# Kernel optimization log

Hardware: AMD Instinct MI355X
Metric: run time of the kernel (lower is better)

Reference implementation:

```python
import jax, jax.numpy as jnp
import numpy as np

N = 50000          # num nodes
E = 800000         # num edges
D = 128            # dim_in == embed_dim
MAX_NODES = 4      # hard-coded in SortConv.__init__
EPS = 1e-5


def setup_inputs() -> dict:
    key = jax.random.key(0)
    ks = jax.random.split(key, 16)
    inp = {
        'x': jax.random.normal(ks[0], (N, D), jnp.float32),
        'edge_index': jax.random.randint(ks[1], (2, E), 0, N, jnp.int32),
    }
    for i in range(2):
        o = 2 + 6 * i
        W = jax.random.normal(ks[o], (D, D), jnp.float32) * (2.0 / (D + D)) ** 0.5
        W = W / jnp.linalg.norm(W, axis=1, keepdims=True)   # reset_parameters row-normalization
        inp[f'W{i}'] = W
        inp[f'b{i}'] = jnp.zeros((D,), jnp.float32)
        inp[f'cw{i}'] = jax.random.normal(ks[o + 1], (MAX_NODES,), jnp.float32) * (2.0 / (MAX_NODES + 1)) ** 0.5
        inp[f'cb{i}'] = jnp.zeros((1,), jnp.float32)
        inp[f'a{i}'] = jax.random.uniform(ks[o + 2], (1,), jnp.float32, -1.0, 1.0)  # LinearCombination scalar
        inp[f'g{i}'] = jnp.ones((D,), jnp.float32)
        inp[f'be{i}'] = jnp.zeros((D,), jnp.float32)
        inp[f'blank{i}'] = jnp.zeros((D,), jnp.float32)      # learnable blank vector
    return inp


def sort_conv(x, edge_index, blank, W, b, cw, cb, a):
    n, d = x.shape
    e = edge_index.shape[1]
    src, dst = edge_index[0], edge_index[1]
    msgs = x[src]                                            # [E, D] raw messages (lin_project not applied to messages)
    order = jnp.argsort(dst)                                 # stable sort by destination (index_sort)
    dst_s = dst[order]
    counts = jax.ops.segment_sum(jnp.ones((e,), jnp.int32), dst, num_segments=n + 1)
    starts = jnp.concatenate([jnp.zeros((1,), jnp.int32), jnp.cumsum(counts)[:-1].astype(jnp.int32)])
    pos = jnp.arange(e, dtype=jnp.int32) - starts[dst_s]     # rank within each neighborhood
    slot = jnp.where(pos < MAX_NODES, pos, MAX_NODES)        # overflow edges -> trash slot (to_dense_batch truncation)
    dense = jnp.zeros((n + 1, MAX_NODES + 1, d), x.dtype).at[dst_s, slot].set(msgs[order])
    mask = jnp.zeros((n + 1, MAX_NODES + 1), bool).at[dst_s, slot].set(True)
    dense, mask = dense[:, :MAX_NODES], mask[:, :MAX_NODES]  # [N+1, 4, D], [N+1, 4]
    blank_p = W @ blank + b                                  # lin_project applied only to blank vector
    filled = dense + (~mask)[..., None].astype(x.dtype) * blank_p
    srt = jnp.sort(filled, axis=1)                           # per-feature sort over neighbor slots
    out = jnp.einsum('nmd,m->nd', srt, cw) + cb              # vector collapse: Linear(max_nodes, 1)
    node_out, blank_new = out[:-1], out[-1]                  # last row = all-blank graph -> new blank
    return a * x + node_out, a * blank + blank_new           # LinearCombination combine (num_repeats=1)


def batch_norm(h, g, be):
    mu = h.mean(0)
    var = h.var(0)
    return (h - mu) / jnp.sqrt(var + EPS) * g + be


def reference(x, edge_index, W0, b0, cw0, cb0, a0, g0, be0, blank0,
              W1, b1, cw1, cb1, a1, g1, be1, blank1):
    layers = [(W0, b0, cw0, cb0, a0, g0, be0, blank0),
              (W1, b1, cw1, cb1, a1, g1, be1, blank1)]
    for (W, b, cw, cb, a, g, be, blank) in layers:
        h, _ = sort_conv(x, edge_index, blank, W, b, cw, cb, a)
        h = batch_norm(h, g, be)
        x = x + h                                            # residual connection
    return x
```

## Files before the change

kernel.cpp:

```cpp
#include <hip/hip_runtime.h>
#include <climits>

constexpr int N_NODES = 50000;
constexpr int N_EDGES = 800000;
constexpr int DIM     = 128;
constexpr int DIM4    = DIM / 4;
constexpr float BN_EPS = 1e-5f;

constexpr int EMPTY = 0x7F7F7F7F;

constexpr int NC = 16;
constexpr int EC = 16;
constexpr int NODES_PER_NC = N_NODES / NC;
constexpr int EDGES_PER_EC = N_EDGES / EC;
constexpr int E4_PER_EC    = EDGES_PER_EC / 4;
constexpr int SEL_THREADS  = 1024;

constexpr int NODES_PER_ITER  = 8;
constexpr int CONV_ITERS      = 2;
constexpr int NODES_PER_BLOCK = NODES_PER_ITER * CONV_ITERS;
constexpr int CONV_GRID = N_NODES / NODES_PER_BLOCK;

constexpr int NBUCKETS = 64;
constexpr int NB_MERGE = (N_NODES + 255) / 256;

__device__ inline float4 f4min(float4 a, float4 b) {
    return make_float4(fminf(a.x,b.x), fminf(a.y,b.y), fminf(a.z,b.z), fminf(a.w,b.w));
}
__device__ inline float4 f4max(float4 a, float4 b) {
    return make_float4(fmaxf(a.x,b.x), fmaxf(a.y,b.y), fmaxf(a.z,b.z), fmaxf(a.w,b.w));
}
__device__ inline float4 f4add(float4 a, float4 b) {
    return make_float4(a.x+b.x, a.y+b.y, a.z+b.z, a.w+b.w);
}
__device__ inline float4 f4fma(float s, float4 v, float4 acc) {
    return make_float4(fmaf(s,v.x,acc.x), fmaf(s,v.y,acc.y), fmaf(s,v.z,acc.z), fmaf(s,v.w,acc.w));
}

__global__ __launch_bounds__(SEL_THREADS)
void select_stageA_kernel(const int* __restrict__ dst,
                          int* __restrict__ tables) {
    __shared__ int slot[NODES_PER_NC * 4];
    const int nc = blockIdx.x & (NC - 1);
    const int ec = blockIdx.x >> 4;
    const int t  = threadIdx.x;

    for (int i = t; i < NODES_PER_NC * 4; i += SEL_THREADS) slot[i] = EMPTY;
    __syncthreads();

    const int r0 = nc * NODES_PER_NC;
    const int4* __restrict__ dst4 = (const int4*)dst;
    const int base4 = ec * E4_PER_EC;
    for (int i = t; i < E4_PER_EC; i += SEL_THREADS) {
        const int4 d = dst4[base4 + i];
        const int ebase = 4 * (base4 + i);
        #define TRY_INS(comp, off) {                                        \
            unsigned n_ = (unsigned)((comp) - r0);                          \
            if (n_ < (unsigned)NODES_PER_NC) {                              \
                int cur_ = ebase + (off);                                   \
                _Pragma("unroll")                                           \
                for (int j_ = 0; j_ < 4; ++j_) {                            \
                    int old_ = atomicMin(&slot[4 * n_ + j_], cur_);         \
                    if (old_ == EMPTY) break;                               \
                    cur_ = max(cur_, old_);                                 \
                } } }
        TRY_INS(d.x, 0); TRY_INS(d.y, 1); TRY_INS(d.z, 2); TRY_INS(d.w, 3);
        #undef TRY_INS
    }
    __syncthreads();

    int4* __restrict__ out = (int4*)tables + (size_t)ec * N_NODES + r0;
    const int4* __restrict__ sl4 = (const int4*)slot;
    for (int n = t; n < NODES_PER_NC; n += SEL_THREADS) out[n] = sl4[n];
}

__global__ __launch_bounds__(256)
void select_stageB_kernel(const int* __restrict__ tables,
                          const int* __restrict__ src,
                          int4* __restrict__ srcs4,
                          float* __restrict__ stats_part,
                          const float* __restrict__ W0, const float* __restrict__ b0,
                          const float* __restrict__ bl0,
                          const float* __restrict__ W1, const float* __restrict__ b1,
                          const float* __restrict__ bl1,
                          float* __restrict__ bp) {
    const int t = threadIdx.x;

    if (blockIdx.x >= NB_MERGE) {
        if (t < DIM) {
            int l = blockIdx.x - NB_MERGE;
            const float* W  = l ? W1  : W0;
            const float* b  = l ? b1  : b0;
            const float* bl = l ? bl1 : bl0;
            float s = 0.f;
            #pragma unroll 8
            for (int j = 0; j < DIM; ++j) s += W[t * DIM + j] * bl[j];
            bp[l * DIM + t] = s + b[t];
        }
        return;
    }

    const int gid = blockIdx.x * 256 + t;
    if (gid < 2 * NBUCKETS * 256) stats_part[gid] = 0.f;

    const int v = gid;
    if (v >= N_NODES) return;

    int b0_ = EMPTY, b1_ = EMPTY, b2_ = EMPTY, b3_ = EMPTY;
    #pragma unroll
    for (int ec = 0; ec < EC; ++ec) {
        const int4 c = ((const int4*)tables)[(size_t)ec * N_NODES + v];
        if (c.x >= b3_) continue;
        #define INS(val) {                                          \
            int x_ = (val);                                         \
            if (x_ < b3_) { b3_ = x_;                               \
                int tm;                                             \
                if (b3_ < b2_) { tm = b2_; b2_ = b3_; b3_ = tm; }   \
                if (b2_ < b1_) { tm = b1_; b1_ = b2_; b2_ = tm; }   \
                if (b1_ < b0_) { tm = b0_; b0_ = b1_; b1_ = tm; } } }
        INS(c.x); INS(c.y); INS(c.z); INS(c.w);
        #undef INS
    }
    int4 o;
    o.x = (b0_ < N_EDGES) ? src[b0_] : -1;
    o.y = (b1_ < N_EDGES) ? src[b1_] : -1;
    o.z = (b2_ < N_EDGES) ? src[b2_] : -1;
    o.w = (b3_ < N_EDGES) ? src[b3_] : -1;
    srcs4[v] = o;
}

__global__ __launch_bounds__(256)
void conv_stats_kernel(const float* __restrict__ x,
                       const int4* __restrict__ srcs4,
                       const float* __restrict__ bp,
                       const float* __restrict__ cw,
                       const float* __restrict__ cb,
                       const float* __restrict__ a,
                       float* __restrict__ h,
                       float* __restrict__ stats_part) {
    const int t    = threadIdx.x;
    const int d4   = t & (DIM4 - 1);
    const int nsub = t >> 5;

    const float4* __restrict__ x4 = (const float4*)x;
    float4*       __restrict__ h4 = (float4*)h;

    const float aa = a[0];
    const float c0 = cw[0], c1 = cw[1], c2 = cw[2], c3 = cw[3];
    const float cbv = cb[0];
    const float4 bpv = ((const float4*)bp)[d4];

    const int v0 = blockIdx.x * NODES_PER_BLOCK + nsub;
    const int v1 = v0 + NODES_PER_ITER;

    const int4 s0 = srcs4[v0];
    const int4 s1 = srcs4[v1];

    float4 g00 = x4[(size_t)max(s0.x, 0) * DIM4 + d4];
    float4 g01 = x4[(size_t)max(s0.y, 0) * DIM4 + d4];
    float4 g02 = x4[(size_t)max(s0.z, 0) * DIM4 + d4];
    float4 g03 = x4[(size_t)max(s0.w, 0) * DIM4 + d4];
    float4 g10 = x4[(size_t)max(s1.x, 0) * DIM4 + d4];
    float4 g11 = x4[(size_t)max(s1.y, 0) * DIM4 + d4];
    float4 g12 = x4[(size_t)max(s1.z, 0) * DIM4 + d4];
    float4 g13 = x4[(size_t)max(s1.w, 0) * DIM4 + d4];
    float4 xv0 = x4[(size_t)v0 * DIM4 + d4];
    float4 xv1 = x4[(size_t)v1 * DIM4 + d4];

    float4 s  = make_float4(0.f, 0.f, 0.f, 0.f);
    float4 s2 = make_float4(0.f, 0.f, 0.f, 0.f);

    #define CSWAP4(p, q) { float4 lo = f4min(p, q); float4 hi = f4max(p, q); p = lo; q = hi; }
    {
        float4 m0 = (s0.x >= 0) ? g00 : bpv;
        float4 m1 = (s0.y >= 0) ? g01 : bpv;
        float4 m2 = (s0.z >= 0) ? g02 : bpv;
        float4 m3 = (s0.w >= 0) ? g03 : bpv;
        CSWAP4(m0, m1); CSWAP4(m2, m3); CSWAP4(m0, m2); CSWAP4(m1, m3); CSWAP4(m1, m2);
        float4 hv = make_float4(cbv, cbv, cbv, cbv);
        hv = f4fma(c0, m0, hv);
        hv = f4fma(c1, m1, hv);
        hv = f4fma(c2, m2, hv);
        hv = f4fma(c3, m3, hv);
        hv = f4fma(aa, xv0, hv);
        h4[(size_t)v0 * DIM4 + d4] = hv;
        s  = f4add(s, hv);
        s2 = f4add(s2, make_float4(hv.x*hv.x, hv.y*hv.y, hv.z*hv.z, hv.w*hv.w));
    }
    {
        float4 m0 = (s1.x >= 0) ? g10 : bpv;
        float4 m1 = (s1.y >= 0) ? g11 : bpv;
        float4 m2 = (s1.z >= 0) ? g12 : bpv;
        float4 m3 = (s1.w >= 0) ? g13 : bpv;
        CSWAP4(m0, m1); CSWAP4(m2, m3); CSWAP4(m0, m2); CSWAP4(m1, m3); CSWAP4(m1, m2);
        float4 hv = make_float4(cbv, cbv, cbv, cbv);
        hv = f4fma(c0, m0, hv);
        hv = f4fma(c1, m1, hv);
        hv = f4fma(c2, m2, hv);
        hv = f4fma(c3, m3, hv);
        hv = f4fma(aa, xv1, hv);
        h4[(size_t)v1 * DIM4 + d4] = hv;
        s  = f4add(s, hv);
        s2 = f4add(s2, make_float4(hv.x*hv.x, hv.y*hv.y, hv.z*hv.z, hv.w*hv.w));
    }
    #undef CSWAP4

    s.x  += __shfl_down(s.x, 32);  s.y  += __shfl_down(s.y, 32);
    s.z  += __shfl_down(s.z, 32);  s.w  += __shfl_down(s.w, 32);
    s2.x += __shfl_down(s2.x, 32); s2.y += __shfl_down(s2.y, 32);
    s2.z += __shfl_down(s2.z, 32); s2.w += __shfl_down(s2.w, 32);

    __shared__ float4 ls[4][32];
    __shared__ float4 ls2[4][32];
    const int wave = t >> 6;
    const int lane = t & 63;
    if (lane < 32) { ls[wave][lane] = s; ls2[wave][lane] = s2; }
    __syncthreads();
    if (t < 32) {
        float* bucket = stats_part + (size_t)(blockIdx.x & (NBUCKETS - 1)) * 256;
        float4 fs  = f4add(f4add(ls[0][t],  ls[1][t]),  f4add(ls[2][t],  ls[3][t]));
        float4 fs2 = f4add(f4add(ls2[0][t], ls2[1][t]), f4add(ls2[2][t], ls2[3][t]));
        atomicAdd(&bucket[4*t + 0], fs.x);
        atomicAdd(&bucket[4*t + 1], fs.y);
        atomicAdd(&bucket[4*t + 2], fs.z);
        atomicAdd(&bucket[4*t + 3], fs.w);
        atomicAdd(&bucket[DIM + 4*t + 0], fs2.x);
        atomicAdd(&bucket[DIM + 4*t + 1], fs2.y);
        atomicAdd(&bucket[DIM + 4*t + 2], fs2.z);
        atomicAdd(&bucket[DIM + 4*t + 3], fs2.w);
    }
}

__global__ void reduce_finalize_kernel(const float* __restrict__ stats_part,
                                       float* __restrict__ final) {
    __shared__ float acc[256];
    int t = threadIdx.x;
    float s = 0.f;
    #pragma unroll 8
    for (int k = 0; k < NBUCKETS; ++k) s += stats_part[k * 256 + t];
    acc[t] = s;
    __syncthreads();
    if (t < 128) {
        constexpr float invN = 1.0f / (float)N_NODES;
        float mu = acc[t] * invN;
        float iv = rsqrtf(acc[128 + t] * invN - mu * mu + BN_EPS);
        final[t]       = mu;
        final[128 + t] = iv;
    }
}

__global__ void bn_apply_kernel(const float* __restrict__ xin,
                                const float* __restrict__ h,
                                const float* __restrict__ final,
                                const float* __restrict__ g,
                                const float* __restrict__ be,
                                float* __restrict__ xout) {
    int idx = blockIdx.x * blockDim.x + threadIdx.x;
    constexpr int TOTAL4 = N_NODES * DIM4;
    if (idx >= TOTAL4) return;
    int d4 = idx & (DIM4 - 1);

    float4 mu = ((const float4*)final)[d4];
    float4 iv = ((const float4*)(final + DIM))[d4];
    float4 hv = ((const float4*)h)[idx];
    float4 xv = ((const float4*)xin)[idx];
    float4 gv = ((const float4*)g)[d4];
    float4 bv = ((const float4*)be)[d4];

    float4 o;
    o.x = xv.x + (hv.x - mu.x) * iv.x * gv.x + bv.x;
    o.y = xv.y + (hv.y - mu.y) * iv.y * gv.y + bv.y;
    o.z = xv.z + (hv.z - mu.z) * iv.z * gv.z + bv.z;
    o.w = xv.w + (hv.w - mu.w) * iv.w * gv.w + bv.w;
    ((float4*)xout)[idx] = o;
}

extern "C" void kernel_launch(void* const* d_in, const int* in_sizes, int n_in,
                              void* d_out, int out_size, void* d_ws, size_t ws_size,
                              hipStream_t stream) {
    const float* x0  = (const float*)d_in[0];
    const int*   ei  = (const int*)d_in[1];
    const int*   src = ei;
    const int*   dst = ei + N_EDGES;

    const float* W[2]; const float* b[2]; const float* cw[2]; const float* cb[2];
    const float* a[2]; const float* g[2]; const float* be[2]; const float* blank[2];
    for (int i = 0; i < 2; ++i) {
        int o = 2 + 8 * i;
        W[i]     = (const float*)d_in[o + 0];
        b[i]     = (const float*)d_in[o + 1];
        cw[i]    = (const float*)d_in[o + 2];
        cb[i]    = (const float*)d_in[o + 3];
        a[i]     = (const float*)d_in[o + 4];
        g[i]     = (const float*)d_in[o + 5];
        be[i]    = (const float*)d_in[o + 6];
        blank[i] = (const float*)d_in[o + 7];
    }

    char* ws = (char*)d_ws;
    int*   srcs       = (int*)ws;
    float* h          = (float*)(srcs + 4 * N_NODES);
    int*   tables     = (int*)h;
    float* stats_part = h + (size_t)N_NODES * DIM;
    float* final_     = stats_part + 2 * NBUCKETS * 256;
    float* bp         = final_ + 512;

    float* xout = (float*)d_out;

    select_stageA_kernel<<<NC * EC, SEL_THREADS, 0, stream>>>(dst, tables);
    select_stageB_kernel<<<NB_MERGE + 2, 256, 0, stream>>>(
        tables, src, (int4*)srcs, stats_part,
        W[0], b[0], blank[0], W[1], b[1], blank[1], bp);

    for (int l = 0; l < 2; ++l) {
        const float* xin = (l == 0) ? x0 : xout;
        float* sp = stats_part + (size_t)l * NBUCKETS * 256;
        conv_stats_kernel<<<CONV_GRID, 256, 0, stream>>>(
            xin, (const int4*)srcs, bp + l * DIM, cw[l], cb[l], a[l], h, sp);
        reduce_finalize_kernel<<<1, 256, 0, stream>>>(sp, final_ + l * 256);
        bn_apply_kernel<<<(N_NODES * DIM4 + 255) / 256, 256, 0, stream>>>(
            xin, h, final_ + l * 256, g[l], be[l], xout);
    }
}
```

Before: 209.7 us.

## Fuse conv, BN statistics and BN apply into one persistent kernel with grid barrier

Replaces the three per-layer kernels (conv+stats, reduce/finalize, bn_apply) with a single persistent kernel of 1024 blocks. Each block keeps its conv outputs in LDS across several tiles. The last block to arrive at an atomic counter reduces the statistics, then releases the other blocks, which apply batch norm straight from LDS. This removes the global write and re-read of the h intermediate and two launches per layer. The trade-off is higher LDS use per block and a spin-wait grid barrier that deadlocks if the 1024 blocks cannot all be resident at once.

```diff
diff --git a/kernel.cpp b/kernel.cpp
--- a/kernel.cpp
+++ b/kernel.cpp
@@ -1,5 +1,4 @@
 #include <hip/hip_runtime.h>
-#include <climits>
 
 constexpr int N_NODES = 50000;
 constexpr int N_EDGES = 800000;
@@ -16,13 +15,16 @@
 constexpr int E4_PER_EC    = EDGES_PER_EC / 4;
 constexpr int SEL_THREADS  = 1024;
 
-constexpr int NODES_PER_ITER  = 8;
-constexpr int CONV_ITERS      = 2;
-constexpr int NODES_PER_BLOCK = NODES_PER_ITER * CONV_ITERS;
-constexpr int CONV_GRID = N_NODES / NODES_PER_BLOCK;
-
-constexpr int NBUCKETS = 64;
+constexpr int NBUCKETS = 32;
 constexpr int NB_MERGE = (N_NODES + 255) / 256;
+
+constexpr int PGRID = 1024;
+constexpr int NODES_PER_TILE = 8;
+constexpr int CONV_GRID = N_NODES / NODES_PER_TILE;
+constexpr int TILES = (CONV_GRID + PGRID - 1) / PGRID;
+
+constexpr int STATS_WORDS = 2 * NBUCKETS * 256;
+constexpr int ZERO_WORDS  = STATS_WORDS + 4;
 
 __device__ inline float4 f4min(float4 a, float4 b) {
     return make_float4(fminf(a.x,b.x), fminf(a.y,b.y), fminf(a.z,b.z), fminf(a.w,b.w));
@@ -101,7 +103,7 @@
     }
 
     const int gid = blockIdx.x * 256 + t;
-    if (gid < 2 * NBUCKETS * 256) stats_part[gid] = 0.f;
+    if (gid < ZERO_WORDS) stats_part[gid] = 0.f;
 
     const int v = gid;
     if (v >= N_NODES) return;
@@ -129,79 +131,70 @@
     srcs4[v] = o;
 }
 
-__global__ __launch_bounds__(256)
-void conv_stats_kernel(const float* __restrict__ x,
-                       const int4* __restrict__ srcs4,
-                       const float* __restrict__ bp,
-                       const float* __restrict__ cw,
-                       const float* __restrict__ cb,
-                       const float* __restrict__ a,
-                       float* __restrict__ h,
-                       float* __restrict__ stats_part) {
+__global__ __launch_bounds__(256, 4)
+void conv_bn_fused_kernel(const float* __restrict__ xin,
+                          const int4* __restrict__ srcs4,
+                          const float* __restrict__ bp,
+                          const float* __restrict__ cw,
+                          const float* __restrict__ cb,
+                          const float* __restrict__ a,
+                          const float* __restrict__ g,
+                          const float* __restrict__ be,
+                          float* __restrict__ stats_part,
+                          float* __restrict__ final_,
+                          int* __restrict__ bar,
+                          float* __restrict__ xout) {
+    __shared__ float4 hv_lds[TILES][256];
+    __shared__ float4 ls[4][32];
+    __shared__ float4 ls2[4][32];
+    __shared__ float acc[256];
+    __shared__ int is_last;
+
     const int t    = threadIdx.x;
+    const int bid  = blockIdx.x;
     const int d4   = t & (DIM4 - 1);
     const int nsub = t >> 5;
 
-    const float4* __restrict__ x4 = (const float4*)x;
-    float4*       __restrict__ h4 = (float4*)h;
+    const float4* __restrict__ x4  = (const float4*)xin;
+    float4*       __restrict__ xo4 = (float4*)xout;
 
     const float aa = a[0];
     const float c0 = cw[0], c1 = cw[1], c2 = cw[2], c3 = cw[3];
     const float cbv = cb[0];
     const float4 bpv = ((const float4*)bp)[d4];
 
-    const int v0 = blockIdx.x * NODES_PER_BLOCK + nsub;
-    const int v1 = v0 + NODES_PER_ITER;
-
-    const int4 s0 = srcs4[v0];
-    const int4 s1 = srcs4[v1];
-
-    float4 g00 = x4[(size_t)max(s0.x, 0) * DIM4 + d4];
-    float4 g01 = x4[(size_t)max(s0.y, 0) * DIM4 + d4];
-    float4 g02 = x4[(size_t)max(s0.z, 0) * DIM4 + d4];
-    float4 g03 = x4[(size_t)max(s0.w, 0) * DIM4 + d4];
-    float4 g10 = x4[(size_t)max(s1.x, 0) * DIM4 + d4];
-    float4 g11 = x4[(size_t)max(s1.y, 0) * DIM4 + d4];
-    float4 g12 = x4[(size_t)max(s1.z, 0) * DIM4 + d4];
-    float4 g13 = x4[(size_t)max(s1.w, 0) * DIM4 + d4];
-    float4 xv0 = x4[(size_t)v0 * DIM4 + d4];
-    float4 xv1 = x4[(size_t)v1 * DIM4 + d4];
-
     float4 s  = make_float4(0.f, 0.f, 0.f, 0.f);
     float4 s2 = make_float4(0.f, 0.f, 0.f, 0.f);
 
     #define CSWAP4(p, q) { float4 lo = f4min(p, q); float4 hi = f4max(p, q); p = lo; q = hi; }
-    {
-        float4 m0 = (s0.x >= 0) ? g00 : bpv;
-        float4 m1 = (s0.y >= 0) ? g01 : bpv;
-        float4 m2 = (s0.z >= 0) ? g02 : bpv;
-        float4 m3 = (s0.w >= 0) ? g03 : bpv;
-        CSWAP4(m0, m1); CSWAP4(m2, m3); CSWAP4(m0, m2); CSWAP4(m1, m3); CSWAP4(m1, m2);
-        float4 hv = make_float4(cbv, cbv, cbv, cbv);
-        hv = f4fma(c0, m0, hv);
-        hv = f4fma(c1, m1, hv);
-        hv = f4fma(c2, m2, hv);
-        hv = f4fma(c3, m3, hv);
-        hv = f4fma(aa, xv0, hv);
-        h4[(size_t)v0 * DIM4 + d4] = hv;
-        s  = f4add(s, hv);
-        s2 = f4add(s2, make_float4(hv.x*hv.x, hv.y*hv.y, hv.z*hv.z, hv.w*hv.w));
-    }
-    {
-        float4 m0 = (s1.x >= 0) ? g10 : bpv;
-        float4 m1 = (s1.y >= 0) ? g11 : bpv;
-        float4 m2 = (s1.z >= 0) ? g12 : bpv;
-        float4 m3 = (s1.w >= 0) ? g13 : bpv;
-        CSWAP4(m0, m1); CSWAP4(m2, m3); CSWAP4(m0, m2); CSWAP4(m1, m3); CSWAP4(m1, m2);
-        float4 hv = make_float4(cbv, cbv, cbv, cbv);
-        hv = f4fma(c0, m0, hv);
-        hv = f4fma(c1, m1, hv);
-        hv = f4fma(c2, m2, hv);
-        hv = f4fma(c3, m3, hv);
-        hv = f4fma(aa, xv1, hv);
-        h4[(size_t)v1 * DIM4 + d4] = hv;
-        s  = f4add(s, hv);
-        s2 = f4add(s2, make_float4(hv.x*hv.x, hv.y*hv.y, hv.z*hv.z, hv.w*hv.w));
+    #pragma unroll
+    for (int k = 0; k < TILES; ++k) {
+        const int tile = k * PGRID + bid;
+        if (tile < CONV_GRID) {
+            const int v = tile * NODES_PER_TILE + nsub;
+            const int4 i0 = srcs4[v];
+
+            float4 g00 = x4[(size_t)max(i0.x, 0) * DIM4 + d4];
+            float4 g01 = x4[(size_t)max(i0.y, 0) * DIM4 + d4];
+            float4 g02 = x4[(size_t)max(i0.z, 0) * DIM4 + d4];
+            float4 g03 = x4[(size_t)max(i0.w, 0) * DIM4 + d4];
+            float4 xv  = x4[(size_t)v * DIM4 + d4];
+
+            float4 m0 = (i0.x >= 0) ? g00 : bpv;
+            float4 m1 = (i0.y >= 0) ? g01 : bpv;
+            float4 m2 = (i0.z >= 0) ? g02 : bpv;
+            float4 m3 = (i0.w >= 0) ? g03 : bpv;
+            CSWAP4(m0, m1); CSWAP4(m2, m3); CSWAP4(m0, m2); CSWAP4(m1, m3); CSWAP4(m1, m2);
+            float4 hv = make_float4(cbv, cbv, cbv, cbv);
+            hv = f4fma(c0, m0, hv);
+            hv = f4fma(c1, m1, hv);
+            hv = f4fma(c2, m2, hv);
+            hv = f4fma(c3, m3, hv);
+            hv = f4fma(aa, xv, hv);
+            hv_lds[k][t] = hv;
+            s  = f4add(s, hv);
+            s2 = f4add(s2, make_float4(hv.x*hv.x, hv.y*hv.y, hv.z*hv.z, hv.w*hv.w));
+        }
     }
     #undef CSWAP4
 
@@ -210,14 +203,12 @@
     s2.x += __shfl_down(s2.x, 32); s2.y += __shfl_down(s2.y, 32);
     s2.z += __shfl_down(s2.z, 32); s2.w += __shfl_down(s2.w, 32);
 
-    __shared__ float4 ls[4][32];
-    __shared__ float4 ls2[4][32];
     const int wave = t >> 6;
     const int lane = t & 63;
     if (lane < 32) { ls[wave][lane] = s; ls2[wave][lane] = s2; }
     __syncthreads();
     if (t < 32) {
-        float* bucket = stats_part + (size_t)(blockIdx.x & (NBUCKETS - 1)) * 256;
+        float* bucket = stats_part + (size_t)(bid & (NBUCKETS - 1)) * 256;
         float4 fs  = f4add(f4add(ls[0][t],  ls[1][t]),  f4add(ls[2][t],  ls[3][t]));
         float4 fs2 = f4add(f4add(ls2[0][t], ls2[1][t]), f4add(ls2[2][t], ls2[3][t]));
         atomicAdd(&bucket[4*t + 0], fs.x);
@@ -229,50 +220,70 @@
         atomicAdd(&bucket[DIM + 4*t + 2], fs2.z);
         atomicAdd(&bucket[DIM + 4*t + 3], fs2.w);
     }
-}
-
-__global__ void reduce_finalize_kernel(const float* __restrict__ stats_part,
-                                       float* __restrict__ final) {
-    __shared__ float acc[256];
-    int t = threadIdx.x;
-    float s = 0.f;
-    #pragma unroll 8
-    for (int k = 0; k < NBUCKETS; ++k) s += stats_part[k * 256 + t];
-    acc[t] = s;
-    __syncthreads();
-    if (t < 128) {
-        constexpr float invN = 1.0f / (float)N_NODES;
-        float mu = acc[t] * invN;
-        float iv = rsqrtf(acc[128 + t] * invN - mu * mu + BN_EPS);
-        final[t]       = mu;
-        final[128 + t] = iv;
-    }
-}
-
-__global__ void bn_apply_kernel(const float* __restrict__ xin,
-                                const float* __restrict__ h,
-                                const float* __restrict__ final,
-                                const float* __restrict__ g,
-                                const float* __restrict__ be,
-                                float* __restrict__ xout) {
-    int idx = blockIdx.x * blockDim.x + threadIdx.x;
-    constexpr int TOTAL4 = N_NODES * DIM4;
-    if (idx >= TOTAL4) return;
-    int d4 = idx & (DIM4 - 1);
-
-    float4 mu = ((const float4*)final)[d4];
-    float4 iv = ((const float4*)(final + DIM))[d4];
-    float4 hv = ((const float4*)h)[idx];
-    float4 xv = ((const float4*)xin)[idx];
-    float4 gv = ((const float4*)g)[d4];
-    float4 bv = ((const float4*)be)[d4];
-
-    float4 o;
-    o.x = xv.x + (hv.x - mu.x) * iv.x * gv.x + bv.x;
-    o.y = xv.y + (hv.y - mu.y) * iv.y * gv.y + bv.y;
-    o.z = xv.z + (hv.z - mu.z) * iv.z * gv.z + bv.z;
-    o.w = xv.w + (hv.w - mu.w) * iv.w * gv.w + bv.w;
-    ((float4*)xout)[idx] = o;
+    __syncthreads();
+
+    if (t == 0) {
+        __threadfence();
+        int arrived = __hip_atomic_fetch_add(&bar[0], 1, __ATOMIC_ACQ_REL,
+                                             __HIP_MEMORY_SCOPE_AGENT);
+        is_last = (arrived == PGRID - 1) ? 1 : 0;
+    }
+    __syncthreads();
+
+    constexpr float invN = 1.0f / (float)N_NODES;
+    if (is_last) {
+        float ssum = 0.f;
+        #pragma unroll 8
+        for (int k2 = 0; k2 < NBUCKETS; ++k2)
+            ssum += __hip_atomic_load(&stats_part[k2 * 256 + t],
+                                      __ATOMIC_RELAXED, __HIP_MEMORY_SCOPE_AGENT);
+        acc[t] = ssum;
+        __syncthreads();
+        if (t < 128) {
+            float mu = acc[t] * invN;
+            float iv = rsqrtf(acc[128 + t] * invN - mu * mu + BN_EPS);
+            acc[t]       = mu;
+            acc[128 + t] = iv;
+            __hip_atomic_store(&final_[t], mu, __ATOMIC_RELAXED, __HIP_MEMORY_SCOPE_AGENT);
+            __hip_atomic_store(&final_[128 + t], iv, __ATOMIC_RELAXED, __HIP_MEMORY_SCOPE_AGENT);
+        }
+        __syncthreads();
+        if (t == 0) {
+            __threadfence();
+            __hip_atomic_store(&bar[1], 1, __ATOMIC_RELEASE, __HIP_MEMORY_SCOPE_AGENT);
+        }
+    } else {
+        if (t == 0) {
+            while (__hip_atomic_load(&bar[1], __ATOMIC_ACQUIRE,
+                                     __HIP_MEMORY_SCOPE_AGENT) == 0)
+                __builtin_amdgcn_s_sleep(2);
+        }
+        __syncthreads();
+        acc[t] = __hip_atomic_load(&final_[t], __ATOMIC_RELAXED, __HIP_MEMORY_SCOPE_AGENT);
+        __syncthreads();
+    }
+
+    const float4 mu4 = make_float4(acc[4*d4+0], acc[4*d4+1], acc[4*d4+2], acc[4*d4+3]);
+    const float4 iv4 = make_float4(acc[128+4*d4+0], acc[128+4*d4+1],
+                                   acc[128+4*d4+2], acc[128+4*d4+3]);
+    const float4 gv = ((const float4*)g)[d4];
+    const float4 bv = ((const float4*)be)[d4];
+
+    #pragma unroll
+    for (int k = 0; k < TILES; ++k) {
+        const int tile = k * PGRID + bid;
+        if (tile < CONV_GRID) {
+            const int v = tile * NODES_PER_TILE + nsub;
+            const float4 xv = x4[(size_t)v * DIM4 + d4];
+            const float4 hv = hv_lds[k][t];
+            float4 o;
+            o.x = xv.x + (hv.x - mu4.x) * iv4.x * gv.x + bv.x;
+            o.y = xv.y + (hv.y - mu4.y) * iv4.y * gv.y + bv.y;
+            o.z = xv.z + (hv.z - mu4.z) * iv4.z * gv.z + bv.z;
+            o.w = xv.w + (hv.w - mu4.w) * iv4.w * gv.w + bv.w;
+            xo4[(size_t)v * DIM4 + d4] = o;
+        }
+    }
 }
 
 extern "C" void kernel_launch(void* const* d_in, const int* in_sizes, int n_in,
@@ -299,10 +310,10 @@
 
     char* ws = (char*)d_ws;
     int*   srcs       = (int*)ws;
-    float* h          = (float*)(srcs + 4 * N_NODES);
-    int*   tables     = (int*)h;
-    float* stats_part = h + (size_t)N_NODES * DIM;
-    float* final_     = stats_part + 2 * NBUCKETS * 256;
+    int*   tables     = srcs + 4 * N_NODES;
+    float* stats_part = (float*)(tables + (size_t)EC * 4 * N_NODES);
+    int*   bar        = (int*)(stats_part + STATS_WORDS);
+    float* final_     = (float*)(bar + 4);
     float* bp         = final_ + 512;
 
     float* xout = (float*)d_out;
@@ -313,12 +324,10 @@
         W[0], b[0], blank[0], W[1], b[1], blank[1], bp);
 
     for (int l = 0; l < 2; ++l) {
-        const float* xin = (l == 0) ? x0 : xout;
-        float* sp = stats_part + (size_t)l * NBUCKETS * 256;
-        conv_stats_kernel<<<CONV_GRID, 256, 0, stream>>>(
-            xin, (const int4*)srcs, bp + l * DIM, cw[l], cb[l], a[l], h, sp);
-        reduce_finalize_kernel<<<1, 256, 0, stream>>>(sp, final_ + l * 256);
-        bn_apply_kernel<<<(N_NODES * DIM4 + 255) / 256, 256, 0, stream>>>(
-            xin, h, final_ + l * 256, g[l], be[l], xout);
-    }
-}
+        const float* xin = (l == 0) ? x0 : (const float*)xout;
+        conv_bn_fused_kernel<<<PGRID, 256, 0, stream>>>(
+            xin, (const int4*)srcs, bp + l * DIM, cw[l], cb[l], a[l],
+            g[l], be[l], stats_part + (size_t)l * NBUCKETS * 256,
+            final_ + l * 256, bar + l * 2, xout);
+    }
+}
```

New measurement: 498.2 us. +137.6%, slower.

## Fuse BN finalize into apply, parallelize top-4 merge, shrink stat buckets

Applied to the files above, without the earlier changes.

The separate single-block reduce/finalize kernel is removed. Each bn_apply block now re-reduces the bucketed partial stats and computes mean and inverse std in shared memory, which saves one launch per layer. Stage B now uses two threads per node: each loads eight tables up front and merges them with sorting-network min/max ops instead of branchy insertion, then the two halves combine through shared memory. NBUCKETS drops from 64 to 16, making the redundant per-block reduction cheaper but putting more atomic contention on each bucket in the conv kernel.

```diff
diff --git a/kernel.cpp b/kernel.cpp
--- a/kernel.cpp
+++ b/kernel.cpp
@@ -1,5 +1,4 @@
 #include <hip/hip_runtime.h>
-#include <climits>
 
 constexpr int N_NODES = 50000;
 constexpr int N_EDGES = 800000;
@@ -16,13 +15,14 @@
 constexpr int E4_PER_EC    = EDGES_PER_EC / 4;
 constexpr int SEL_THREADS  = 1024;
 
+constexpr int NBUCKETS = 16;
+constexpr int ZERO_WORDS = 2 * NBUCKETS * 256;
+
+constexpr int NB_MERGE = (N_NODES + 127) / 128;
+
 constexpr int NODES_PER_ITER  = 8;
-constexpr int CONV_ITERS      = 2;
-constexpr int NODES_PER_BLOCK = NODES_PER_ITER * CONV_ITERS;
+constexpr int NODES_PER_BLOCK = 16;
 constexpr int CONV_GRID = N_NODES / NODES_PER_BLOCK;
-
-constexpr int NBUCKETS = 64;
-constexpr int NB_MERGE = (N_NODES + 255) / 256;
 
 __device__ inline float4 f4min(float4 a, float4 b) {
     return make_float4(fminf(a.x,b.x), fminf(a.y,b.y), fminf(a.z,b.z), fminf(a.w,b.w));
@@ -101,32 +101,46 @@
     }
 
     const int gid = blockIdx.x * 256 + t;
-    if (gid < 2 * NBUCKETS * 256) stats_part[gid] = 0.f;
-
-    const int v = gid;
-    if (v >= N_NODES) return;
-
-    int b0_ = EMPTY, b1_ = EMPTY, b2_ = EMPTY, b3_ = EMPTY;
+    if (gid < ZERO_WORDS) stats_part[gid] = 0.f;
+
+    const int vloc = t & 127;
+    const int half = t >> 7;
+    int v = blockIdx.x * 128 + vloc;
+    const bool valid = (v < N_NODES);
+    if (!valid) v = N_NODES - 1;
+
+    int4 c[8];
     #pragma unroll
-    for (int ec = 0; ec < EC; ++ec) {
-        const int4 c = ((const int4*)tables)[(size_t)ec * N_NODES + v];
-        if (c.x >= b3_) continue;
-        #define INS(val) {                                          \
-            int x_ = (val);                                         \
-            if (x_ < b3_) { b3_ = x_;                               \
-                int tm;                                             \
-                if (b3_ < b2_) { tm = b2_; b2_ = b3_; b3_ = tm; }   \
-                if (b2_ < b1_) { tm = b1_; b1_ = b2_; b2_ = tm; }   \
-                if (b1_ < b0_) { tm = b0_; b0_ = b1_; b1_ = tm; } } }
-        INS(c.x); INS(c.y); INS(c.z); INS(c.w);
-        #undef INS
-    }
-    int4 o;
-    o.x = (b0_ < N_EDGES) ? src[b0_] : -1;
-    o.y = (b1_ < N_EDGES) ? src[b1_] : -1;
-    o.z = (b2_ < N_EDGES) ? src[b2_] : -1;
-    o.w = (b3_ < N_EDGES) ? src[b3_] : -1;
-    srcs4[v] = o;
+    for (int j = 0; j < 8; ++j)
+        c[j] = ((const int4*)tables)[(size_t)(half * 8 + j) * N_NODES + v];
+
+    int a0 = c[0].x, a1 = c[0].y, a2 = c[0].z, a3 = c[0].w;
+    #define MERGE4(cx, cy, cz, cw) {                                 \
+        int m0 = min(a0, (cw)), m1 = min(a1, (cz));                  \
+        int m2 = min(a2, (cy)), m3 = min(a3, (cx));                  \
+        int u_;                                                      \
+        u_ = min(m0, m2); m2 = max(m0, m2); m0 = u_;                 \
+        u_ = min(m1, m3); m3 = max(m1, m3); m1 = u_;                 \
+        u_ = min(m0, m1); m1 = max(m0, m1); m0 = u_;                 \
+        u_ = min(m2, m3); m3 = max(m2, m3); m2 = u_;                 \
+        a0 = m0; a1 = m1; a2 = m2; a3 = m3; }
+    #pragma unroll
+    for (int j = 1; j < 8; ++j) MERGE4(c[j].x, c[j].y, c[j].z, c[j].w);
+
+    __shared__ int4 xbuf[128];
+    if (half) xbuf[vloc] = make_int4(a0, a1, a2, a3);
+    __syncthreads();
+    if (!half) {
+        const int4 o = xbuf[vloc];
+        MERGE4(o.x, o.y, o.z, o.w);
+        int4 r;
+        r.x = (a0 < N_EDGES) ? src[a0] : -1;
+        r.y = (a1 < N_EDGES) ? src[a1] : -1;
+        r.z = (a2 < N_EDGES) ? src[a2] : -1;
+        r.w = (a3 < N_EDGES) ? src[a3] : -1;
+        if (valid) srcs4[v] = r;
+    }
+    #undef MERGE4
 }
 
 __global__ __launch_bounds__(256)
@@ -231,47 +245,46 @@
     }
 }
 
-__global__ void reduce_finalize_kernel(const float* __restrict__ stats_part,
-                                       float* __restrict__ final) {
+__global__ __launch_bounds__(256)
+void bn_apply_kernel(const float* __restrict__ xin,
+                     const float* __restrict__ h,
+                     const float* __restrict__ stats_part,
+                     const float* __restrict__ g,
+                     const float* __restrict__ be,
+                     float* __restrict__ xout) {
     __shared__ float acc[256];
-    int t = threadIdx.x;
-    float s = 0.f;
-    #pragma unroll 8
-    for (int k = 0; k < NBUCKETS; ++k) s += stats_part[k * 256 + t];
-    acc[t] = s;
+    const int t = threadIdx.x;
+
+    float ssum = 0.f;
+    #pragma unroll
+    for (int k = 0; k < NBUCKETS; ++k) ssum += stats_part[k * 256 + t];
+    acc[t] = ssum;
     __syncthreads();
     if (t < 128) {
         constexpr float invN = 1.0f / (float)N_NODES;
         float mu = acc[t] * invN;
         float iv = rsqrtf(acc[128 + t] * invN - mu * mu + BN_EPS);
-        final[t]       = mu;
-        final[128 + t] = iv;
-    }
-}
-
-__global__ void bn_apply_kernel(const float* __restrict__ xin,
-                                const float* __restrict__ h,
-                                const float* __restrict__ final,
-                                const float* __restrict__ g,
-                                const float* __restrict__ be,
-                                float* __restrict__ xout) {
-    int idx = blockIdx.x * blockDim.x + threadIdx.x;
-    constexpr int TOTAL4 = N_NODES * DIM4;
-    if (idx >= TOTAL4) return;
-    int d4 = idx & (DIM4 - 1);
-
-    float4 mu = ((const float4*)final)[d4];
-    float4 iv = ((const float4*)(final + DIM))[d4];
-    float4 hv = ((const float4*)h)[idx];
-    float4 xv = ((const float4*)xin)[idx];
-    float4 gv = ((const float4*)g)[d4];
-    float4 bv = ((const float4*)be)[d4];
+        acc[t]       = mu;
+        acc[128 + t] = iv;
+    }
+    __syncthreads();
+
+    const int idx = blockIdx.x * 256 + t;
+    const int d4 = idx & (DIM4 - 1);
+
+    const float4 mu4 = make_float4(acc[4*d4+0], acc[4*d4+1], acc[4*d4+2], acc[4*d4+3]);
+    const float4 iv4 = make_float4(acc[128+4*d4+0], acc[128+4*d4+1],
+                                   acc[128+4*d4+2], acc[128+4*d4+3]);
+    const float4 hv = ((const float4*)h)[idx];
+    const float4 xv = ((const float4*)xin)[idx];
+    const float4 gv = ((const float4*)g)[d4];
+    const float4 bv = ((const float4*)be)[d4];
 
     float4 o;
-    o.x = xv.x + (hv.x - mu.x) * iv.x * gv.x + bv.x;
-    o.y = xv.y + (hv.y - mu.y) * iv.y * gv.y + bv.y;
-    o.z = xv.z + (hv.z - mu.z) * iv.z * gv.z + bv.z;
-    o.w = xv.w + (hv.w - mu.w) * iv.w * gv.w + bv.w;
+    o.x = xv.x + (hv.x - mu4.x) * iv4.x * gv.x + bv.x;
+    o.y = xv.y + (hv.y - mu4.y) * iv4.y * gv.y + bv.y;
+    o.z = xv.z + (hv.z - mu4.z) * iv4.z * gv.z + bv.z;
+    o.w = xv.w + (hv.w - mu4.w) * iv4.w * gv.w + bv.w;
     ((float4*)xout)[idx] = o;
 }
 
@@ -302,8 +315,7 @@
     float* h          = (float*)(srcs + 4 * N_NODES);
     int*   tables     = (int*)h;
     float* stats_part = h + (size_t)N_NODES * DIM;
-    float* final_     = stats_part + 2 * NBUCKETS * 256;
-    float* bp         = final_ + 512;
+    float* bp         = stats_part + ZERO_WORDS;
 
     float* xout = (float*)d_out;
 
@@ -317,8 +329,7 @@
         float* sp = stats_part + (size_t)l * NBUCKETS * 256;
         conv_stats_kernel<<<CONV_GRID, 256, 0, stream>>>(
             xin, (const int4*)srcs, bp + l * DIM, cw[l], cb[l], a[l], h, sp);
-        reduce_finalize_kernel<<<1, 256, 0, stream>>>(sp, final_ + l * 256);
-        bn_apply_kernel<<<(N_NODES * DIM4 + 255) / 256, 256, 0, stream>>>(
-            xin, h, final_ + l * 256, g[l], be[l], xout);
-    }
-}
+        bn_apply_kernel<<<(N_NODES * DIM4) / 256, 256, 0, stream>>>(
+            xin, h, sp, g[l], be[l], xout);
+    }
+}
```

Result: no change. 207.2 us (-1.2%).
